# Optimization experiments

Measured on AMD Instinct MI355X. Metric: run time of the kernel, lower is better.

## Reference

```python
import jax, jax.numpy as jnp
import numpy as np

N, E, G = 50000, 800000, 64        # nodes, edges, graphs in batch
IN, HID, OUT = 64, 128, 8


def gcn_conv(x, W, b, src, dst, num_nodes):
    """GCNConv: h = D^-1/2 (A+I) D^-1/2 (x W) + b, self-loops already in src/dst."""
    h = x @ W                                              # [N, out]
    deg = jax.ops.segment_sum(jnp.ones_like(dst, dtype=h.dtype), dst,
                              num_segments=num_nodes)      # [N]
    dinv = jax.lax.rsqrt(jnp.maximum(deg, 1.0))
    norm = dinv[src] * dinv[dst]                           # [E+N]
    msg = h[src] * norm[:, None]                           # gather + scale
    out = jax.ops.segment_sum(msg, dst, num_segments=num_nodes)
    return out + b


def global_mean_pool(x, batch, num_graphs):
    s = jax.ops.segment_sum(x, batch, num_segments=num_graphs)
    cnt = jax.ops.segment_sum(jnp.ones((x.shape[0],), x.dtype), batch,
                              num_segments=num_graphs)
    return s / jnp.maximum(cnt, 1.0)[:, None]


def setup_inputs() -> dict:
    key = jax.random.key(0)
    ks = jax.random.split(key, 11)
    def glorot(k, fi, fo):
        return jax.random.normal(k, (fi, fo), jnp.float32) * np.float32(1.0 / np.sqrt(fi))
    return {
        "x": jax.random.normal(ks[0], (N, IN), jnp.float32),
        "W1": glorot(ks[1], IN, HID),  "b1": jnp.zeros((HID,), jnp.float32),
        "W2": glorot(ks[2], HID, HID), "b2": jnp.zeros((HID,), jnp.float32),
        "W3": glorot(ks[3], HID, HID), "b3": jnp.zeros((HID,), jnp.float32),
        "Wh": glorot(ks[4], HID, OUT), "bh": jnp.zeros((OUT,), jnp.float32),
        "edge_index": jax.random.randint(ks[5], (2, E), 0, N),
        "batch": jnp.sort(jax.random.randint(ks[6], (N,), 0, G)),
    }


def reference(x, W1, b1, W2, b2, W3, b3, Wh, bh, edge_index, batch):
    loops = jnp.arange(N, dtype=edge_index.dtype)
    src = jnp.concatenate([edge_index[0], loops])          # add self-loops
    dst = jnp.concatenate([edge_index[1], loops])
    h = jax.nn.relu(gcn_conv(x, W1, b1, src, dst, N))
    h = jax.nn.relu(gcn_conv(h, W2, b2, src, dst, N))
    h = gcn_conv(h, W3, b3, src, dst, N)
    g = global_mean_pool(h, batch, G)                      # [G, HID]
    return g @ Wh + bh                                     # [G, OUT]
```

## Files before the change

### kernel.cpp

```cpp
#include <hip/hip_runtime.h>

typedef short bf8_t __attribute__((ext_vector_type(8)));
typedef float f32x4 __attribute__((ext_vector_type(4)));
typedef unsigned short u16;

__device__ inline u16 f2bf(float f) {
    unsigned u = __float_as_uint(f);
    return (u16)((u + 0x7fff + ((u >> 16) & 1)) >> 16);
}


__global__ void deg_kernel(const int* __restrict__ dst, int* __restrict__ deg,
                           u16* __restrict__ rank, int E) {
    int e = blockIdx.x * 256 + threadIdx.x;
    if (e < E) rank[e] = (u16)atomicAdd(&deg[dst[e]], 1);
}

__global__ void scan_blocksum(const int* __restrict__ deg, int* __restrict__ bsum,
                              float* __restrict__ dinv, int n) {
    int i = blockIdx.x * 256 + threadIdx.x;
    int d = (i < n) ? (deg[i] + 1) : 0;
    if (i < n) dinv[i] = rsqrtf((float)d);
    int v = (i < n) ? ((d + 7) & ~7) : 0;
    for (int off = 32; off > 0; off >>= 1) v += __shfl_down(v, off, 64);
    __shared__ int ws[4];
    if ((threadIdx.x & 63) == 0) ws[threadIdx.x >> 6] = v;
    __syncthreads();
    if (threadIdx.x == 0) bsum[blockIdx.x] = ws[0] + ws[1] + ws[2] + ws[3];
}

__global__ void scan_offsets(const int* __restrict__ bsum, int* __restrict__ boff, int nblk) {
    __shared__ int buf[256];
    int tid = threadIdx.x;
    int v = (tid < nblk) ? bsum[tid] : 0;
    buf[tid] = v;
    __syncthreads();
    for (int off = 1; off < 256; off <<= 1) {
        int t = (tid >= off) ? buf[tid - off] : 0;
        __syncthreads();
        buf[tid] += t;
        __syncthreads();
    }
    if (tid < nblk) boff[tid] = buf[tid] - v;
}

__global__ void scan_rowptr(const int* __restrict__ deg, const int* __restrict__ boff,
                            int* __restrict__ row_ptr, int n) {
    __shared__ int buf[256];
    int tid = threadIdx.x;
    int i = blockIdx.x * 256 + tid;
    int v = (i < n) ? ((deg[i] + 8) & ~7) : 0;
    buf[tid] = v;
    __syncthreads();
    for (int off = 1; off < 256; off <<= 1) {
        int t = (tid >= off) ? buf[tid - off] : 0;
        __syncthreads();
        buf[tid] += t;
        __syncthreads();
    }
    int excl = buf[tid] - v + boff[blockIdx.x];
    if (i < n) row_ptr[i] = excl;
    if (i == n - 1) row_ptr[n] = excl + v;
}


__global__ void prep_kernel(const int* __restrict__ src, const int* __restrict__ dst,
                            const u16* __restrict__ rank, const int* __restrict__ row_ptr,
                            const int* __restrict__ deg,
                            u16* __restrict__ csr_src,
                            const float* __restrict__ x, const float* __restrict__ dinv,
                            unsigned* __restrict__ x16, unsigned* __restrict__ h16a,
                            unsigned* __restrict__ h16b,
                            const float* __restrict__ W1, const float* __restrict__ W2,
                            const float* __restrict__ W3,
                            const float* __restrict__ Wh, const float* __restrict__ b3,
                            const float* __restrict__ bh,
                            u16* __restrict__ Wt1, u16* __restrict__ Wt2,
                            float* __restrict__ WhF, float* __restrict__ bhF,
                            int E, int n, int total8) {
    int gid = blockIdx.x * 256 + threadIdx.x;
    if (gid < E) {
        int s = src[gid], d = dst[gid];
        int pos = row_ptr[d] + 1 + (int)rank[gid];
        __builtin_nontemporal_store((u16)s, &csr_src[pos]);
        return;
    }
    if (gid < E + n) {
        int s = gid - E;
        int beg = row_ptr[s];
        csr_src[beg] = (u16)s;
        int fill0 = beg + deg[s] + 1, fill1 = row_ptr[s + 1];
        for (int p = fill0; p < fill1; ++p) csr_src[p] = (u16)n;
        return;
    }
    int i = gid - (E + n);
    if (i < total8) {
        float dn = dinv[i >> 3];
        const float4* x4 = (const float4*)x;
        float4 a = x4[i * 2], b = x4[i * 2 + 1];
        uint4 o;
        o.x = (unsigned)f2bf(a.x * dn) | ((unsigned)f2bf(a.y * dn) << 16);
        o.y = (unsigned)f2bf(a.z * dn) | ((unsigned)f2bf(a.w * dn) << 16);
        o.z = (unsigned)f2bf(b.x * dn) | ((unsigned)f2bf(b.y * dn) << 16);
        o.w = (unsigned)f2bf(b.z * dn) | ((unsigned)f2bf(b.w * dn) << 16);
        ((uint4*)x16)[i] = o;
        return;
    }
    int j = i - total8;
    if (j < 8192) {
        int nn = j / 64, k = j - nn * 64;
        Wt1[j] = f2bf(W1[k * 128 + nn]);
        return;
    }
    if (j < 24576) {
        int jj = j - 8192;
        int nn = jj / 128, k = jj - nn * 128;
        Wt2[jj] = f2bf(W2[k * 128 + nn]);
        return;
    }
    if (j < 25600) {
        int jj = j - 24576;
        int k = jj >> 3, o = jj & 7;
        float a = 0.f;
        for (int q = 0; q < 128; ++q)
            a += W3[k * 128 + q] * Wh[q * 8 + o];
        WhF[jj] = a;
        return;
    }
    if (j < 25608) {
        int o = j - 25600;
        float a = bh[o];
        for (int q = 0; q < 128; ++q)
            a += b3[q] * Wh[q * 8 + o];
        bhF[o] = a;
        return;
    }
    int z = j - 25608;
    if (z < 8)       ((uint4*)x16) [(size_t)n * 8  + z]        = make_uint4(0, 0, 0, 0);
    else if (z < 24) ((uint4*)h16a)[(size_t)n * 16 + (z - 8)]  = make_uint4(0, 0, 0, 0);
    else if (z < 40) ((uint4*)h16b)[(size_t)n * 16 + (z - 24)] = make_uint4(0, 0, 0, 0);
}


__device__ inline void bf8_add(uint4 a, float* acc) {
#pragma unroll
    for (int j = 0; j < 4; ++j) {
        unsigned u = ((const unsigned*)&a)[j];
        acc[2 * j]     += __uint_as_float(u << 16);
        acc[2 * j + 1] += __uint_as_float(u & 0xffff0000u);
    }
}

__device__ inline uint4 pack_bf8(const float* v, float dn) {
    uint4 o;
    o.x = (unsigned)f2bf(v[0] * dn) | ((unsigned)f2bf(v[1] * dn) << 16);
    o.y = (unsigned)f2bf(v[2] * dn) | ((unsigned)f2bf(v[3] * dn) << 16);
    o.z = (unsigned)f2bf(v[4] * dn) | ((unsigned)f2bf(v[5] * dn) << 16);
    o.w = (unsigned)f2bf(v[6] * dn) | ((unsigned)f2bf(v[7] * dn) << 16);
    return o;
}


template<int K, bool RELU, bool BF16OUT>
__global__ __launch_bounds__(256) void agg_gemm(
        const u16* __restrict__ in, const u16* __restrict__ Wt16,
        const float* __restrict__ bias, void* __restrict__ outp,
        const int* __restrict__ row_ptr, const u16* __restrict__ csr_src,
        const float* __restrict__ dinv, int n) {
    constexpr int KS = K / 32;
    __shared__ u16 As[16 * K];
    int w = threadIdx.x >> 6, lane = threadIdx.x & 63;
    int base = blockIdx.x * 16;
    int lr = lane & 15, lk = lane >> 4;

    bf8_t B[2][KS];
#pragma unroll
    for (int f = 0; f < 2; ++f) {
        int col = w * 32 + f * 16 + lr;
#pragma unroll
        for (int ks = 0; ks < KS; ++ks)
            B[f][ks] = *reinterpret_cast<const bf8_t*>(&Wt16[(size_t)col * K + ks * 32 + lk * 8]);
    }

    const uint4* in4 = (const uint4*)in;
    int g = lane >> 4;
    int row = w * 4 + g;
    int node = base + row;
    float acc[8] = {0.f, 0.f, 0.f, 0.f, 0.f, 0.f, 0.f, 0.f};

    if (K == 128) {
        int col = lane & 15;
        if (node < n) {
            int beg = row_ptr[node];
            int niter = (row_ptr[node + 1] - beg) >> 3;
            const uint4* idxp = (const uint4*)(csr_src + beg);
            uint4 iv = idxp[0];
            for (int it = 0; it < niter; ++it) {
                uint4 ivn = idxp[it + 1];
                int s0 = iv.x & 0xffff, s1 = iv.x >> 16;
                int s2 = iv.y & 0xffff, s3 = iv.y >> 16;
                int s4 = iv.z & 0xffff, s5 = iv.z >> 16;
                int s6 = iv.w & 0xffff, s7 = iv.w >> 16;
                uint4 a0 = in4[(size_t)s0 * 16 + col];
                uint4 a1 = in4[(size_t)s1 * 16 + col];
                uint4 a2 = in4[(size_t)s2 * 16 + col];
                uint4 a3 = in4[(size_t)s3 * 16 + col];
                bf8_add(a0, acc); bf8_add(a1, acc);
                bf8_add(a2, acc); bf8_add(a3, acc);
                uint4 a4 = in4[(size_t)s4 * 16 + col];
                uint4 a5 = in4[(size_t)s5 * 16 + col];
                uint4 a6 = in4[(size_t)s6 * 16 + col];
                uint4 a7 = in4[(size_t)s7 * 16 + col];
                bf8_add(a4, acc); bf8_add(a5, acc);
                bf8_add(a6, acc); bf8_add(a7, acc);
                iv = ivn;
            }
        }
        float dn = (node < n) ? dinv[node] : 0.f;
        int off = row * K + ((col * 8) ^ ((row & 7) << 3));
        *(uint4*)&As[off] = pack_bf8(acc, dn);
    } else {
        int sub = (lane >> 3) & 1;
        int col = lane & 7;
        if (node < n) {
            int beg = row_ptr[node];
            int niter = (row_ptr[node + 1] - beg) >> 3;
            const uint4* idxp = (const uint4*)(csr_src + beg);
            uint4 iv = idxp[0];
            for (int it = 0; it < niter; ++it) {
                uint4 ivn = idxp[it + 1];
                int e0 = sub ? (int)(iv.x >> 16) : (int)(iv.x & 0xffff);
                int e1 = sub ? (int)(iv.y >> 16) : (int)(iv.y & 0xffff);
                int e2 = sub ? (int)(iv.z >> 16) : (int)(iv.z & 0xffff);
                int e3 = sub ? (int)(iv.w >> 16) : (int)(iv.w & 0xffff);
                uint4 a0 = in4[(size_t)e0 * 8 + col];
                uint4 a1 = in4[(size_t)e1 * 8 + col];
                uint4 a2 = in4[(size_t)e2 * 8 + col];
                uint4 a3 = in4[(size_t)e3 * 8 + col];
                bf8_add(a0, acc); bf8_add(a1, acc);
                bf8_add(a2, acc); bf8_add(a3, acc);
                iv = ivn;
            }
        }
#pragma unroll
        for (int j = 0; j < 8; ++j)
            acc[j] += __shfl_xor(acc[j], 8, 64);
        if (sub == 0) {
            float dn = (node < n) ? dinv[node] : 0.f;
            int off = row * K + ((col * 8) ^ ((row & 7) << 3));
            *(uint4*)&As[off] = pack_bf8(acc, dn);
        }
    }
    __syncthreads();

    f32x4 pacc[2] = {};
#pragma unroll
    for (int ks = 0; ks < KS; ++ks) {
        int off = lr * K + (((ks * 32) + lk * 8) ^ ((lr & 7) << 3));
        bf8_t a = *reinterpret_cast<const bf8_t*>(&As[off]);
#pragma unroll
        for (int f = 0; f < 2; ++f)
            pacc[f] = __builtin_amdgcn_mfma_f32_16x16x32_bf16(B[f][ks], a, pacc[f], 0, 0, 0);
    }

    int orow = base + lr;
    if (orow < n) {
        float dnx = BF16OUT ? dinv[orow] : 1.f;
#pragma unroll
        for (int f = 0; f < 2; ++f) {
            int c0 = w * 32 + f * 16 + lk * 4;
            float4 bv = *(const float4*)&bias[c0];
            float v0 = pacc[f][0] + bv.x, v1 = pacc[f][1] + bv.y;
            float v2 = pacc[f][2] + bv.z, v3 = pacc[f][3] + bv.w;
            if (RELU) {
                v0 = fmaxf(v0, 0.f); v1 = fmaxf(v1, 0.f);
                v2 = fmaxf(v2, 0.f); v3 = fmaxf(v3, 0.f);
            }
            if (BF16OUT) {
                uint2 o;
                o.x = (unsigned)f2bf(v0 * dnx) | ((unsigned)f2bf(v1 * dnx) << 16);
                o.y = (unsigned)f2bf(v2 * dnx) | ((unsigned)f2bf(v3 * dnx) << 16);
                *(uint2*)&((u16*)outp)[(size_t)orow * 128 + c0] = o;
            } else {
                *(float4*)&((float*)outp)[(size_t)orow * 128 + c0] = make_float4(v0, v1, v2, v3);
            }
        }
    }
}


__global__ __launch_bounds__(256) void agg_only(
        const u16* __restrict__ in, u16* __restrict__ out,
        const int* __restrict__ row_ptr, const u16* __restrict__ csr_src,
        const float* __restrict__ dinv, int n) {
    int lane = threadIdx.x & 63;
    int w = threadIdx.x >> 6;
    int node = blockIdx.x * 16 + w * 4 + (lane >> 4);
    int col = lane & 15;
    if (node >= n) return;
    const uint4* in4 = (const uint4*)in;
    float acc[8] = {0.f, 0.f, 0.f, 0.f, 0.f, 0.f, 0.f, 0.f};
    int beg = row_ptr[node];
    int niter = (row_ptr[node + 1] - beg) >> 3;
    const uint4* idxp = (const uint4*)(csr_src + beg);
    uint4 iv = idxp[0];
    for (int it = 0; it < niter; ++it) {
        uint4 ivn = idxp[it + 1];
        int s0 = iv.x & 0xffff, s1 = iv.x >> 16;
        int s2 = iv.y & 0xffff, s3 = iv.y >> 16;
        int s4 = iv.z & 0xffff, s5 = iv.z >> 16;
        int s6 = iv.w & 0xffff, s7 = iv.w >> 16;
        uint4 a0 = in4[(size_t)s0 * 16 + col];
        uint4 a1 = in4[(size_t)s1 * 16 + col];
        uint4 a2 = in4[(size_t)s2 * 16 + col];
        uint4 a3 = in4[(size_t)s3 * 16 + col];
        bf8_add(a0, acc); bf8_add(a1, acc);
        bf8_add(a2, acc); bf8_add(a3, acc);
        uint4 a4 = in4[(size_t)s4 * 16 + col];
        uint4 a5 = in4[(size_t)s5 * 16 + col];
        uint4 a6 = in4[(size_t)s6 * 16 + col];
        uint4 a7 = in4[(size_t)s7 * 16 + col];
        bf8_add(a4, acc); bf8_add(a5, acc);
        bf8_add(a6, acc); bf8_add(a7, acc);
        iv = ivn;
    }
    ((uint4*)out)[(size_t)node * 16 + col] = pack_bf8(acc, dinv[node]);
}


__device__ inline int lbound(const int* __restrict__ batch, int n, int g) {
    int lo = 0, hi = n;
    while (lo < hi) {
        int mid = (lo + hi) >> 1;
        if (batch[mid] < g) lo = mid + 1; else hi = mid;
    }
    return lo;
}

#define PSPLIT 16
__global__ __launch_bounds__(256) void pool_part(
        const u16* __restrict__ v, const int* __restrict__ batch,
        float* __restrict__ part, int n) {
    int g = blockIdx.x >> 4, sp = blockIdx.x & (PSPLIT - 1);
    int tid = threadIdx.x;
    int c2 = tid & 63;
    int rs = tid >> 6;
    int beg = lbound(batch, n, g), end = lbound(batch, n, g + 1);
    int len = end - beg;
    int chunk = (len + PSPLIT - 1) >> 4;
    int r0 = beg + sp * chunk;
    int r1 = min(r0 + chunk, end);
    const unsigned* v32 = (const unsigned*)v;
    float ax = 0.f, ay = 0.f;
    for (int r = r0 + rs; r < r1; r += 4) {
        unsigned u = v32[(size_t)r * 64 + c2];
        ax += __uint_as_float(u << 16);
        ay += __uint_as_float(u & 0xffff0000u);
    }
    __shared__ float bufx[256], bufy[256];
    bufx[tid] = ax; bufy[tid] = ay;
    __syncthreads();
    if (rs == 0) {
        float sx = bufx[c2] + bufx[c2 + 64] + bufx[c2 + 128] + bufx[c2 + 192];
        float sy = bufy[c2] + bufy[c2 + 64] + bufy[c2 + 128] + bufy[c2 + 192];
        part[(size_t)blockIdx.x * 128 + c2 * 2]     = sx;
        part[(size_t)blockIdx.x * 128 + c2 * 2 + 1] = sy;
    }
}

__global__ __launch_bounds__(128) void pool_head(
        const float* __restrict__ part, const int* __restrict__ batch,
        const float* __restrict__ WhF, const float* __restrict__ bhF,
        float* __restrict__ out, int n) {
    int g = blockIdx.x;
    int tid = threadIdx.x;
    float acc = 0.f;
#pragma unroll
    for (int sp = 0; sp < PSPLIT; ++sp)
        acc += part[((size_t)g * PSPLIT + sp) * 128 + tid];
    int cnt = lbound(batch, n, g + 1) - lbound(batch, n, g);
    __shared__ float grow[128];
    grow[tid] = acc / fmaxf((float)cnt, 1.f);
    __syncthreads();
    int sub = tid >> 3, o = tid & 7;
    float p = 0.f;
    for (int k = sub; k < 128; k += 16)
        p += grow[k] * WhF[k * 8 + o];
    __shared__ float p2[128];
    p2[tid] = p;
    __syncthreads();
    for (int s = 8; s > 0; s >>= 1) {
        if (sub < s) p2[sub * 8 + o] += p2[(sub + s) * 8 + o];
        __syncthreads();
    }
    if (tid < 8) out[g * 8 + tid] = p2[tid] + bhF[tid];
}


extern "C" void kernel_launch(void* const* d_in, const int* in_sizes, int n_in,
                              void* d_out, int out_size, void* d_ws, size_t ws_size,
                              hipStream_t stream) {
    const float* x  = (const float*)d_in[0];
    const float* W1 = (const float*)d_in[1];
    const float* b1 = (const float*)d_in[2];
    const float* W2 = (const float*)d_in[3];
    const float* b2 = (const float*)d_in[4];
    const float* W3 = (const float*)d_in[5];
    const float* b3 = (const float*)d_in[6];
    const float* Wh = (const float*)d_in[7];
    const float* bh = (const float*)d_in[8];
    const int* edge_index = (const int*)d_in[9];
    const int* batch = (const int*)d_in[10];
    (void)n_in; (void)ws_size;

    const int N = in_sizes[10];
    const int E = in_sizes[9] / 2;
    const int G = out_size / 8;
    const int* esrc = edge_index;
    const int* edst = edge_index + E;

    size_t off = 0;
    auto take = [&](size_t bytes) {
        void* p = (char*)d_ws + off;
        off += (bytes + 255) & ~(size_t)255;
        return p;
    };
    int*   deg      = (int*)take((size_t)N * 4);
    float* dinv     = (float*)take((size_t)N * 4);
    int*   row_ptr  = (int*)take((size_t)(N + 1) * 4);
    u16*   rank     = (u16*)take((size_t)E * 2);
    u16*   csr_src  = (u16*)take(((size_t)E + 8 * (size_t)N + 16) * 2);
    int*   bsum     = (int*)take(256 * 4);
    int*   boff     = (int*)take(256 * 4);
    float* part     = (float*)take((size_t)G * PSPLIT * 128 * 4);
    u16*   x16      = (u16*)take((size_t)(N + 1) * 64 * 2);
    u16*   h16a     = (u16*)take((size_t)(N + 1) * 128 * 2);
    u16*   h16b     = (u16*)take((size_t)(N + 1) * 128 * 2);
    u16*   vbuf     = (u16*)take((size_t)N * 128 * 2);
    u16*   Wt1      = (u16*)take((size_t)128 * 64 * 2);
    u16*   Wt2      = (u16*)take((size_t)128 * 128 * 2);
    float* WhF      = (float*)take((size_t)128 * 8 * 4);
    float* bhF      = (float*)take(8 * 4);

    int nblk  = (N + 255) / 256;
    int fgrid = (N + 15) / 16;
    int total8 = N * 64 / 8;
    int prep_threads = E + N + total8 + 25608 + 40;

    hipMemsetAsync(deg, 0, (size_t)N * 4, stream);

    deg_kernel<<<(E + 255) / 256, 256, 0, stream>>>(edst, deg, rank, E);
    scan_blocksum<<<nblk, 256, 0, stream>>>(deg, bsum, dinv, N);
    scan_offsets<<<1, 256, 0, stream>>>(bsum, boff, nblk);
    scan_rowptr<<<nblk, 256, 0, stream>>>(deg, boff, row_ptr, N);
    prep_kernel<<<(prep_threads + 255) / 256, 256, 0, stream>>>(
        esrc, edst, rank, row_ptr, deg, csr_src, x, dinv,
        (unsigned*)x16, (unsigned*)h16a, (unsigned*)h16b,
        W1, W2, W3, Wh, b3, bh, Wt1, Wt2, WhF, bhF, E, N, total8);

    agg_gemm<64,  true, true><<<fgrid, 256, 0, stream>>>(x16,  Wt1, b1, h16a, row_ptr, csr_src, dinv, N);
    agg_gemm<128, true, true><<<fgrid, 256, 0, stream>>>(h16a, Wt2, b2, h16b, row_ptr, csr_src, dinv, N);
    agg_only<<<fgrid, 256, 0, stream>>>(h16b, vbuf, row_ptr, csr_src, dinv, N);

    pool_part<<<G * PSPLIT, 256, 0, stream>>>(vbuf, batch, part, N);
    pool_head<<<G, 128, 0, stream>>>(part, batch, WhF, bhF, (float*)d_out, N);
}
```

Measured before the change: 189.0 us.

## Build CSR via two-level bucket sort instead of global atomic degree counting

Replaces the global-atomic degree count and random scatter into CSR with a two-pass bucket sort. Edges are first histogrammed into 256-node buckets per 2048-edge block using shared-memory atomics, then scattered into a bucket-ordered buffer. Per-bucket kernels then compute node degrees and ranks with shared atomics and write csr_src locally. This targets contended global atomics and scattered writes, at the cost of four extra launches, a serial single-block prefix over all edge blocks, and an extra edge buffer pass.

```diff
diff --git a/kernel.cpp b/kernel.cpp
--- a/kernel.cpp
+++ b/kernel.cpp
@@ -9,12 +9,92 @@
     return (u16)((u + 0x7fff + ((u >> 16) & 1)) >> 16);
 }
 
-
-__global__ void deg_kernel(const int* __restrict__ dst, int* __restrict__ deg,
-                           u16* __restrict__ rank, int E) {
-    int e = blockIdx.x * 256 + threadIdx.x;
-    if (e < E) rank[e] = (u16)atomicAdd(&deg[dst[e]], 1);
-}
+#define EBLK 2048
+
+__global__ __launch_bounds__(256) void bkt_hist(
+        const int* __restrict__ dst, int* __restrict__ bcnt,
+        u16* __restrict__ lrank1, int E) {
+    __shared__ int bins[256];
+    int tid = threadIdx.x;
+    bins[tid] = 0;
+    __syncthreads();
+    int base = blockIdx.x * EBLK;
+    int end = min(base + EBLK, E);
+    for (int e = base + tid; e < end; e += 256) {
+        int b = dst[e] >> 8;
+        lrank1[e] = (u16)atomicAdd(&bins[b], 1);
+    }
+    __syncthreads();
+    bcnt[blockIdx.x * 256 + tid] = bins[tid];
+}
+
+__global__ __launch_bounds__(256) void bkt_prefix(
+        int* __restrict__ bcnt, int* __restrict__ bbase, int nebk) {
+    int b = threadIdx.x;
+    int run = 0;
+#pragma unroll 4
+    for (int k = 0; k < nebk; ++k) {
+        int t = bcnt[k * 256 + b];
+        bcnt[k * 256 + b] = run;
+        run += t;
+    }
+    __shared__ int tot[256];
+    tot[b] = run;
+    __syncthreads();
+    if (b == 0) {
+        int r = 0;
+        for (int k = 0; k < 256; ++k) { bbase[k] = r; r += tot[k]; }
+        bbase[256] = r;
+    }
+}
+
+__global__ __launch_bounds__(256) void bkt_scatter(
+        const int* __restrict__ src, const int* __restrict__ dst,
+        const u16* __restrict__ lrank1, const int* __restrict__ bcnt,
+        const int* __restrict__ bbase, unsigned* __restrict__ ebuf, int E) {
+    int base = blockIdx.x * EBLK;
+    int end = min(base + EBLK, E);
+    for (int e = base + threadIdx.x; e < end; e += 256) {
+        int d = dst[e];
+        int b = d >> 8;
+        int pos = bbase[b] + bcnt[blockIdx.x * 256 + b] + (int)lrank1[e];
+        unsigned v = (unsigned)src[e] | ((unsigned)(d & 255) << 16);
+        __builtin_nontemporal_store(v, &ebuf[pos]);
+    }
+}
+
+__global__ __launch_bounds__(256) void bkt_nodehist(
+        const unsigned* __restrict__ ebuf, const int* __restrict__ bbase,
+        int* __restrict__ deg, u16* __restrict__ lrank2, int n) {
+    __shared__ int hist[256];
+    int tid = threadIdx.x;
+    hist[tid] = 0;
+    __syncthreads();
+    int b = blockIdx.x;
+    int s0 = bbase[b], s1 = bbase[b + 1];
+    for (int i = s0 + tid; i < s1; i += 256) {
+        unsigned u = ebuf[i];
+        lrank2[i] = (u16)atomicAdd(&hist[u >> 16], 1);
+    }
+    __syncthreads();
+    int node = b * 256 + tid;
+    if (node < n) deg[node] = hist[tid];
+}
+
+__global__ __launch_bounds__(256) void bkt_fill(
+        const unsigned* __restrict__ ebuf, const int* __restrict__ bbase,
+        const u16* __restrict__ lrank2, const int* __restrict__ row_ptr,
+        u16* __restrict__ csr_src, int n) {
+    int b = blockIdx.x;
+    int s0 = bbase[b], s1 = bbase[b + 1];
+    for (int i = s0 + threadIdx.x; i < s1; i += 256) {
+        unsigned u = ebuf[i];
+        int node = b * 256 + (int)(u >> 16);
+        int pos = row_ptr[node] + 1 + (int)lrank2[i];
+        __builtin_nontemporal_store((u16)(u & 0xffffu), &csr_src[pos]);
+    }
+}
+
 
 __global__ void scan_blocksum(const int* __restrict__ deg, int* __restrict__ bsum,
                               float* __restrict__ dinv, int n) {
@@ -64,9 +144,7 @@
 }
 
 
-__global__ void prep_kernel(const int* __restrict__ src, const int* __restrict__ dst,
-                            const u16* __restrict__ rank, const int* __restrict__ row_ptr,
-                            const int* __restrict__ deg,
+__global__ void prep_kernel(const int* __restrict__ row_ptr, const int* __restrict__ deg,
                             u16* __restrict__ csr_src,
                             const float* __restrict__ x, const float* __restrict__ dinv,
                             unsigned* __restrict__ x16, unsigned* __restrict__ h16a,
@@ -77,23 +155,17 @@
                             const float* __restrict__ bh,
                             u16* __restrict__ Wt1, u16* __restrict__ Wt2,
                             float* __restrict__ WhF, float* __restrict__ bhF,
-                            int E, int n, int total8) {
+                            int n, int total8) {
     int gid = blockIdx.x * 256 + threadIdx.x;
-    if (gid < E) {
-        int s = src[gid], d = dst[gid];
-        int pos = row_ptr[d] + 1 + (int)rank[gid];
-        __builtin_nontemporal_store((u16)s, &csr_src[pos]);
-        return;
-    }
-    if (gid < E + n) {
-        int s = gid - E;
+    if (gid < n) {
+        int s = gid;
         int beg = row_ptr[s];
         csr_src[beg] = (u16)s;
         int fill0 = beg + deg[s] + 1, fill1 = row_ptr[s + 1];
         for (int p = fill0; p < fill1; ++p) csr_src[p] = (u16)n;
         return;
     }
-    int i = gid - (E + n);
+    int i = gid - n;
     if (i < total8) {
         float dn = dinv[i >> 3];
         const float4* x4 = (const float4*)x;
@@ -425,10 +497,16 @@
         off += (bytes + 255) & ~(size_t)255;
         return p;
     };
+    int nebk = (E + EBLK - 1) / EBLK;
+    int NB   = (N + 255) >> 8;
     int*   deg      = (int*)take((size_t)N * 4);
     float* dinv     = (float*)take((size_t)N * 4);
     int*   row_ptr  = (int*)take((size_t)(N + 1) * 4);
-    u16*   rank     = (u16*)take((size_t)E * 2);
+    u16*   lrank1   = (u16*)take((size_t)E * 2);
+    u16*   lrank2   = (u16*)take((size_t)E * 2);
+    unsigned* ebuf  = (unsigned*)take((size_t)E * 4);
+    int*   bcnt     = (int*)take((size_t)nebk * 256 * 4);
+    int*   bbase    = (int*)take(257 * 4);
     u16*   csr_src  = (u16*)take(((size_t)E + 8 * (size_t)N + 16) * 2);
     int*   bsum     = (int*)take(256 * 4);
     int*   boff     = (int*)take(256 * 4);
@@ -445,18 +523,20 @@
     int nblk  = (N + 255) / 256;
     int fgrid = (N + 15) / 16;
     int total8 = N * 64 / 8;
-    int prep_threads = E + N + total8 + 25608 + 40;
-
-    hipMemsetAsync(deg, 0, (size_t)N * 4, stream);
-
-    deg_kernel<<<(E + 255) / 256, 256, 0, stream>>>(edst, deg, rank, E);
+    int prep_threads = N + total8 + 25608 + 40;
+
+    bkt_hist<<<nebk, 256, 0, stream>>>(edst, bcnt, lrank1, E);
+    bkt_prefix<<<1, 256, 0, stream>>>(bcnt, bbase, nebk);
+    bkt_scatter<<<nebk, 256, 0, stream>>>(esrc, edst, lrank1, bcnt, bbase, ebuf, E);
+    bkt_nodehist<<<NB, 256, 0, stream>>>(ebuf, bbase, deg, lrank2, N);
     scan_blocksum<<<nblk, 256, 0, stream>>>(deg, bsum, dinv, N);
     scan_offsets<<<1, 256, 0, stream>>>(bsum, boff, nblk);
     scan_rowptr<<<nblk, 256, 0, stream>>>(deg, boff, row_ptr, N);
+    bkt_fill<<<NB, 256, 0, stream>>>(ebuf, bbase, lrank2, row_ptr, csr_src, N);
     prep_kernel<<<(prep_threads + 255) / 256, 256, 0, stream>>>(
-        esrc, edst, rank, row_ptr, deg, csr_src, x, dinv,
+        row_ptr, deg, csr_src, x, dinv,
         (unsigned*)x16, (unsigned*)h16a, (unsigned*)h16b,
-        W1, W2, W3, Wh, b3, bh, Wt1, Wt2, WhF, bhF, E, N, total8);
+        W1, W2, W3, Wh, b3, bh, Wt1, Wt2, WhF, bhF, N, total8);
 
     agg_gemm<64,  true, true><<<fgrid, 256, 0, stream>>>(x16,  Wt1, b1, h16a, row_ptr, csr_src, dinv, N);
     agg_gemm<128, true, true><<<fgrid, 256, 0, stream>>>(h16a, Wt2, b2, h16b, row_ptr, csr_src, dinv, N);
```

Measured after the change: 204.9 us. +8.4%, slower.
